# Performance work log

Measured on AMD Instinct MI355X. Metric: run time of the kernel, lower is better.

## Reference

```python
import jax, jax.numpy as jnp
import numpy as np
from math import pi

EPS = 1e-7
GAIN = 3.5  # weight_logits_softmax_gain
MAX_LOG_VAR = 3.5


def _upper_triangular(v, T, K, D):
    # replicate tf concat([v, v[...,::-1], zeros[...,D]], axis=2) -> reshape [T,K,D,D] -> strict-upper mask
    zero_pad = jnp.zeros((T, K, D), dtype=v.dtype)
    a_flat = jnp.concatenate([v, v[..., ::-1], zero_pad], axis=2)
    a = a_flat.reshape(T, K, D, D)
    idx = jnp.arange(D)
    mask = (idx[:, None] < idx[None, :]).astype(v.dtype)
    return a * mask[None, None, :, :]


def _diag_transforms(cov_param, T, K, D):
    ut = _upper_triangular(cov_param, T, K, D)
    a = 0.5 * (jnp.swapaxes(ut, -1, -2) - ut)  # antisymmetric [T,K,D,D]
    eye = jnp.eye(D, dtype=cov_param.dtype)[None, None]
    q = jnp.matmul(eye - a, jnp.linalg.inv(eye + a))  # Cayley transform
    return q


def setup_inputs() -> dict:
    key = jax.random.key(0)
    k1, k2, k3, k4, k5 = jax.random.split(key, 5)
    B, T, K, D = 2048, 512, 8, 8
    x = jax.random.normal(k1, (B, T, D), dtype=jnp.float32)
    kernel_centers = jax.random.uniform(k2, (T, K, D), dtype=jnp.float32)
    weight_logits = jax.random.normal(k3, (T, K), dtype=jnp.float32)
    log_variance = jax.random.normal(k4, (T, K, D), dtype=jnp.float32)
    cov_param = jax.random.normal(k5, (T, K, D * (D - 1) // 2), dtype=jnp.float32)
    return {"x": x, "kernel_centers": kernel_centers, "weight_logits": weight_logits,
            "log_variance": log_variance, "cov_param": cov_param}


def reference(x, kernel_centers, weight_logits, log_variance, cov_param):
    T, K, D = kernel_centers.shape
    # subtract kernel centers: [B,T,K,D]
    xc = x[:, :, None, :] - kernel_centers[None]
    # covariance-diagonalizing rotation (Cayley transform of antisym matrix)
    q = _diag_transforms(cov_param, T, K, D)  # [T,K,D,D]
    xt = jnp.einsum('btki,tkij->btkj', xc, q)
    # per-dimension Gaussian pdf
    var = jnp.exp(jnp.clip(log_variance, -MAX_LOG_VAR, MAX_LOG_VAR))[None]  # [1,T,K,D]
    norm_coeff = 1.0 / jnp.sqrt(2.0 * pi * var)
    gaussians = norm_coeff * jnp.exp(-0.5 * xt * xt / var)  # [B,T,K,D]
    # mix: product over dims (in log space), weighted sum over kernels
    lgpe = jnp.sum(jnp.log(gaussians + EPS), axis=-1)  # [B,T,K]
    p_kernels = jnp.exp(lgpe)
    w = jax.nn.softmax(jnp.clip(weight_logits, -GAIN, GAIN), axis=-1)  # [T,K]
    p = jnp.sum(p_kernels * w[None], axis=-1)  # [B,T]
    return p
```

## Files before the change

### kernel.cpp

```cpp
#include <hip/hip_runtime.h>
#include <math.h>

#define TDIM 512
#define KDIM 8
#define DDIM 8
#define BDIM 2048

#define PSTRIDE 76
#define XSTRIDE 132

#ifndef __has_builtin
#define __has_builtin(x) 0
#endif
#if __has_builtin(__builtin_amdgcn_exp2f)
#define FAST_EXP2(x) __builtin_amdgcn_exp2f(x)
#else
#define FAST_EXP2(x) exp2f(x)
#endif

__global__ __launch_bounds__(512) void precompute_kernel(
    const float* __restrict__ centers,
    const float* __restrict__ wlogits,
    const float* __restrict__ logvar,
    const float* __restrict__ covp,
    float* __restrict__ P)
{
    const int tid = (int)blockIdx.x * 512 + (int)threadIdx.x;
    const int tk  = tid >> 3;
    const int r   = tid & 7;
    const size_t tkg = (size_t)tk;

    const float* cb = covp + tkg * 28;
    float row[8];
    #pragma unroll
    for (int j = 0; j < 8; j++) {
        const int lo = (r < j) ? r : j;
        const int hi = (r < j) ? j : r;
        const int n  = 8 * lo + hi;
        const int m  = (r == j) ? 0 : ((n < 28) ? n : 55 - n);
        const float v = cb[m];
        const float a = (r < j) ? -0.5f * v : 0.5f * v;
        row[j] = (r == j) ? 1.0f : a;
    }

    #pragma unroll
    for (int c = 0; c < 8; c++) {
        float prow[8];
        #pragma unroll
        for (int j = 0; j < 8; j++) prow[j] = __shfl(row[j], c, 8);
        const float pinv = 1.0f / prow[c];
        const float f = row[c];
        #pragma unroll
        for (int j = 0; j < 8; j++) {
            if (j == c) {
                row[j] = (r == c) ? pinv : -f * pinv;
            } else {
                const float spiv = prow[j] * pinv;
                row[j] = (r == c) ? spiv : fmaf(-f, spiv, row[j]);
            }
        }
    }

    const float* lvp = logvar + tkg * 8;
    float invstd[8];
    float sumlv = 0.0f;
    #pragma unroll
    for (int j = 0; j < 8; j++) {
        const float lv = fminf(fmaxf(lvp[j], -3.5f), 3.5f);
        sumlv += lv;
        invstd[j] = exp2f(lv * -0.7213475204444817f);
    }
    const float cr = centers[tkg * 8 + r];
    float* pp = P + tkg * PSTRIDE;
    float offp[8];
    #pragma unroll
    for (int j = 0; j < 8; j++) {
        const float q = 2.0f * row[j] - (r == j ? 1.0f : 0.0f);
        const float val = q * (invstd[j] * 0.8493218002880191f);
        pp[j * 8 + r] = val;
        offp[j] = cr * val;
    }
    #pragma unroll
    for (int j = 0; j < 8; j++) {
        offp[j] += __shfl_xor(offp[j], 1, 8);
        offp[j] += __shfl_xor(offp[j], 2, 8);
        offp[j] += __shfl_xor(offp[j], 4, 8);
    }

    float l = fminf(fmaxf(wlogits[tkg], -3.5f), 3.5f);
    float mx = l;
    mx = fmaxf(mx, __shfl_xor(mx, 8, 64));
    mx = fmaxf(mx, __shfl_xor(mx, 16, 64));
    mx = fmaxf(mx, __shfl_xor(mx, 32, 64));
    const float e = exp2f((l - mx) * 1.4426950408889634f);
    float ss = e;
    ss += __shfl_xor(ss, 8, 64);
    ss += __shfl_xor(ss, 16, 64);
    ss += __shfl_xor(ss, 32, 64);
    const float log2w = (l - mx) * 1.4426950408889634f - log2f(ss);

    if (r == 0) {
        #pragma unroll
        for (int j = 0; j < 8; j++) pp[64 + j] = offp[j];
        pp[72] = log2w - 10.605984517349169f - 0.7213475204444817f * sumlv;
    }
}

__global__ __launch_bounds__(512, 8) void pecd_main(
    const float* __restrict__ x,
    const float* __restrict__ P,
    float* __restrict__ out)
{
    __shared__ float xs[64 * XSTRIDE];

    const int tidx = (int)threadIdx.x;
    const int wv   = tidx >> 6;
    const int ln   = tidx & 63;
    const int t0   = (int)blockIdx.x * 16;
    const int b0   = (int)blockIdx.y * 64;

    #pragma unroll
    for (int it = 0; it < 4; it++) {
        const int idx = tidx + it * 512;
        const int row = idx >> 5;
        const int col = idx & 31;
        const float4 v =
            *((const float4*)(x + ((size_t)(b0 + row) * TDIM + t0) * DDIM) + col);
        *(float4*)(xs + row * XSTRIDE + col * 4) = v;
    }
    __syncthreads();

    float xv[2][8];
    #pragma unroll
    for (int tt = 0; tt < 2; tt++) {
        const float* xr = xs + ln * XSTRIDE + (wv * 2 + tt) * 8;
        const float4 a0 = *(const float4*)(xr);
        const float4 a1 = *(const float4*)(xr + 4);
        xv[tt][0] = a0.x; xv[tt][1] = a0.y; xv[tt][2] = a0.z; xv[tt][3] = a0.w;
        xv[tt][4] = a1.x; xv[tt][5] = a1.y; xv[tt][6] = a1.z; xv[tt][7] = a1.w;
    }

    float accs[2];
    #pragma unroll
    for (int tt = 0; tt < 2; tt++) {
        const int ts = __builtin_amdgcn_readfirstlane(t0 + wv * 2 + tt);
        const float* __restrict__ pt = P + (size_t)ts * (KDIM * PSTRIDE);
        float acc = 0.0f;
        #pragma unroll 1
        for (int k = 0; k < KDIM; k++) {
            const float* pk = pt + k * PSTRIDE;
            float s0 = 0.0f, s1 = 0.0f;
            #pragma unroll
            for (int j = 0; j < 8; j++) {
                float u = -pk[64 + j];
                #pragma unroll
                for (int i = 0; i < 8; i++) u = fmaf(xv[tt][i], pk[j * 8 + i], u);
                if (j & 1) s1 = fmaf(u, u, s1);
                else       s0 = fmaf(u, u, s0);
            }
            acc += FAST_EXP2(pk[72] - s0 - s1);
        }
        accs[tt] = acc;
    }

    __syncthreads();
    xs[ln * 18 + wv * 2 + 0] = accs[0];
    xs[ln * 18 + wv * 2 + 1] = accs[1];
    __syncthreads();
    {
        const int row = tidx >> 3;
        const int col = tidx & 7;
        const float2 v = *(const float2*)&xs[row * 18 + col * 2];
        *(float2*)(out + (size_t)(b0 + row) * TDIM + t0 + col * 2) = v;
    }
}

extern "C" void kernel_launch(void* const* d_in, const int* in_sizes, int n_in,
                              void* d_out, int out_size, void* d_ws, size_t ws_size,
                              hipStream_t stream) {
    const float* x       = (const float*)d_in[0];
    const float* centers = (const float*)d_in[1];
    const float* wlogits = (const float*)d_in[2];
    const float* logvar  = (const float*)d_in[3];
    const float* covp    = (const float*)d_in[4];
    float* out = (float*)d_out;

    float* P = (float*)d_ws;

    precompute_kernel<<<dim3(TDIM * KDIM * 8 / 512), dim3(512), 0, stream>>>(
        centers, wlogits, logvar, covp, P);

    dim3 grid(TDIM / 16, BDIM / 64);
    pecd_main<<<grid, dim3(512), 0, stream>>>(x, P, out);
}
```

Before: 103.0 us.

## Replace rotated-distance matmul with symmetric quadratic form in main kernel

The precompute kernel now builds the symmetric matrix S = Q diag(1/(2var)) Q^T per kernel and stores only its upper triangle, a linear term and a constant (48 floats instead of 76). The main kernel then evaluates a quadratic form x^T S x + lin·x + c with about 44 FMAs per kernel instead of 72, using four partial accumulators. The k loop is also unrolled by two. Expanding the quadratic instead of squaring centered differences can lose precision when the exponent is large.

```diff
diff --git a/kernel.cpp b/kernel.cpp
--- a/kernel.cpp
+++ b/kernel.cpp
@@ -6,7 +6,7 @@
 #define DDIM 8
 #define BDIM 2048
 
-#define PSTRIDE 76
+#define PSTRIDE 48
 #define XSTRIDE 132
 
 #ifndef __has_builtin
@@ -60,32 +60,44 @@
             }
         }
     }
+    float qr[8];
+    #pragma unroll
+    for (int j = 0; j < 8; j++) qr[j] = 2.0f * row[j] - (r == j ? 1.0f : 0.0f);
 
     const float* lvp = logvar + tkg * 8;
-    float invstd[8];
+    float sc2[8];
     float sumlv = 0.0f;
     #pragma unroll
     for (int j = 0; j < 8; j++) {
         const float lv = fminf(fmaxf(lvp[j], -3.5f), 3.5f);
         sumlv += lv;
-        invstd[j] = exp2f(lv * -0.7213475204444817f);
-    }
-    const float cr = centers[tkg * 8 + r];
-    float* pp = P + tkg * PSTRIDE;
-    float offp[8];
-    #pragma unroll
-    for (int j = 0; j < 8; j++) {
-        const float q = 2.0f * row[j] - (r == j ? 1.0f : 0.0f);
-        const float val = q * (invstd[j] * 0.8493218002880191f);
-        pp[j * 8 + r] = val;
-        offp[j] = cr * val;
-    }
-    #pragma unroll
-    for (int j = 0; j < 8; j++) {
-        offp[j] += __shfl_xor(offp[j], 1, 8);
-        offp[j] += __shfl_xor(offp[j], 2, 8);
-        offp[j] += __shfl_xor(offp[j], 4, 8);
-    }
+        sc2[j] = 0.7213475204444817f * exp2f(lv * -1.4426950408889634f);
+    }
+    float w[8];
+    #pragma unroll
+    for (int j = 0; j < 8; j++) w[j] = qr[j] * sc2[j];
+
+    float Srow[8];
+    #pragma unroll
+    for (int m = 0; m < 8; m++) {
+        float s = 0.0f;
+        #pragma unroll
+        for (int j = 0; j < 8; j++) s = fmaf(w[j], __shfl(qr[j], m, 8), s);
+        Srow[m] = s;
+    }
+
+    const float* cp = centers + tkg * 8;
+    float cvec[8];
+    #pragma unroll
+    for (int m = 0; m < 8; m++) cvec[m] = cp[m];
+    float tr = 0.0f;
+    #pragma unroll
+    for (int m = 0; m < 8; m++) tr = fmaf(Srow[m], cvec[m], tr);
+    const float lin = -2.0f * tr;
+    float cpart = cp[r] * tr;
+    cpart += __shfl_xor(cpart, 1, 8);
+    cpart += __shfl_xor(cpart, 2, 8);
+    cpart += __shfl_xor(cpart, 4, 8);
 
     float l = fminf(fmaxf(wlogits[tkg], -3.5f), 3.5f);
     float mx = l;
@@ -98,12 +110,16 @@
     ss += __shfl_xor(ss, 16, 64);
     ss += __shfl_xor(ss, 32, 64);
     const float log2w = (l - mx) * 1.4426950408889634f - log2f(ss);
-
-    if (r == 0) {
-        #pragma unroll
-        for (int j = 0; j < 8; j++) pp[64 + j] = offp[j];
-        pp[72] = log2w - 10.605984517349169f - 0.7213475204444817f * sumlv;
-    }
+    const float slc = log2w - 10.605984517349169f - 0.7213475204444817f * sumlv;
+
+    float* pp = P + tkg * PSTRIDE;
+    const int o = 9 * r - (r * (r - 1)) / 2;
+    pp[o] = lin;
+    #pragma unroll
+    for (int j = 0; j < 8; j++) {
+        if (j >= r) pp[o + 1 + j - r] = Srow[j] * ((j == r) ? 1.0f : 2.0f);
+    }
+    if (r == 0) pp[44] = cpart - slc;
 }
 
 __global__ __launch_bounds__(512, 8) void pecd_main(
@@ -122,43 +138,43 @@
     #pragma unroll
     for (int it = 0; it < 4; it++) {
         const int idx = tidx + it * 512;
-        const int row = idx >> 5;
-        const int col = idx & 31;
+        const int rowi = idx >> 5;
+        const int col  = idx & 31;
         const float4 v =
-            *((const float4*)(x + ((size_t)(b0 + row) * TDIM + t0) * DDIM) + col);
-        *(float4*)(xs + row * XSTRIDE + col * 4) = v;
+            *((const float4*)(x + ((size_t)(b0 + rowi) * TDIM + t0) * DDIM) + col);
+        *(float4*)(xs + rowi * XSTRIDE + col * 4) = v;
     }
     __syncthreads();
 
-    float xv[2][8];
+    float accs[2];
     #pragma unroll
     for (int tt = 0; tt < 2; tt++) {
+        const int ts = __builtin_amdgcn_readfirstlane(t0 + wv * 2 + tt);
+        const float* __restrict__ pt = P + (size_t)ts * (KDIM * PSTRIDE);
+
         const float* xr = xs + ln * XSTRIDE + (wv * 2 + tt) * 8;
         const float4 a0 = *(const float4*)(xr);
         const float4 a1 = *(const float4*)(xr + 4);
-        xv[tt][0] = a0.x; xv[tt][1] = a0.y; xv[tt][2] = a0.z; xv[tt][3] = a0.w;
-        xv[tt][4] = a1.x; xv[tt][5] = a1.y; xv[tt][6] = a1.z; xv[tt][7] = a1.w;
-    }
-
-    float accs[2];
-    #pragma unroll
-    for (int tt = 0; tt < 2; tt++) {
-        const int ts = __builtin_amdgcn_readfirstlane(t0 + wv * 2 + tt);
-        const float* __restrict__ pt = P + (size_t)ts * (KDIM * PSTRIDE);
+        const float xv[8] = {a0.x, a0.y, a0.z, a0.w, a1.x, a1.y, a1.z, a1.w};
+
         float acc = 0.0f;
-        #pragma unroll 1
+        #pragma unroll 2
         for (int k = 0; k < KDIM; k++) {
             const float* pk = pt + k * PSTRIDE;
-            float s0 = 0.0f, s1 = 0.0f;
+            float e0 = pk[44], e1 = 0.0f, e2 = 0.0f, e3 = 0.0f;
             #pragma unroll
-            for (int j = 0; j < 8; j++) {
-                float u = -pk[64 + j];
+            for (int i = 0; i < 8; i++) {
+                const int o = 9 * i - (i * (i - 1)) / 2;
+                float inner = pk[o];
                 #pragma unroll
-                for (int i = 0; i < 8; i++) u = fmaf(xv[tt][i], pk[j * 8 + i], u);
-                if (j & 1) s1 = fmaf(u, u, s1);
-                else       s0 = fmaf(u, u, s0);
+                for (int j = i; j < 8; j++)
+                    inner = fmaf(pk[o + 1 + j - i], xv[j], inner);
+                if ((i & 3) == 0)      e0 = fmaf(xv[i], inner, e0);
+                else if ((i & 3) == 1) e1 = fmaf(xv[i], inner, e1);
+                else if ((i & 3) == 2) e2 = fmaf(xv[i], inner, e2);
+                else                   e3 = fmaf(xv[i], inner, e3);
             }
-            acc += FAST_EXP2(pk[72] - s0 - s1);
+            acc += FAST_EXP2(-((e0 + e1) + (e2 + e3)));
         }
         accs[tt] = acc;
     }
@@ -168,10 +184,10 @@
     xs[ln * 18 + wv * 2 + 1] = accs[1];
     __syncthreads();
     {
-        const int row = tidx >> 3;
-        const int col = tidx & 7;
-        const float2 v = *(const float2*)&xs[row * 18 + col * 2];
-        *(float2*)(out + (size_t)(b0 + row) * TDIM + t0 + col * 2) = v;
+        const int rowi = tidx >> 3;
+        const int col  = tidx & 7;
+        const float2 v = *(const float2*)&xs[rowi * 18 + col * 2];
+        *(float2*)(out + (size_t)(b0 + rowi) * TDIM + t0 + col * 2) = v;
     }
 }
 
```

Result: faster. 96.40 us (-6.4%).
